# Performance work log

Hardware: AMD Instinct MI355X
Metric: run time of the kernel (lower is better)

The kernel has to match this reference:

```python
import jax, jax.numpy as jnp
import numpy as np

H = 32          # num query heads
KV = 8          # num kv heads
D = 64          # head_dim
WIN = 512       # sliding_window
BASE = 10000.0  # rope base


def setup_inputs() -> dict:
    key = jax.random.key(0)
    ks = jax.random.split(key, 5)
    B, S, DIM = 2, 2048, 2048
    x = jax.random.normal(ks[0], (B, S, DIM), dtype=jnp.float32)
    wq = jax.random.normal(ks[1], (H * D, DIM), dtype=jnp.float32) * 0.02
    wk = jax.random.normal(ks[2], (KV * D, DIM), dtype=jnp.float32) * 0.02
    wv = jax.random.normal(ks[3], (KV * D, DIM), dtype=jnp.float32) * 0.02
    wo = jax.random.normal(ks[4], (DIM, H * D), dtype=jnp.float32) * 0.02
    return {"x": x, "wq": wq, "wk": wk, "wv": wv, "wo": wo}


def _rope_tables(S):
    inv_freq = 1.0 / (BASE ** (jnp.arange(0, D, 2, dtype=jnp.float32) / D))
    t = jnp.arange(S, dtype=jnp.float32)
    freqs = t[:, None] * inv_freq[None, :]          # [S, D/2]
    emb = jnp.concatenate([freqs, freqs], axis=-1)  # [S, D]
    return jnp.cos(emb)[:, None, :], jnp.sin(emb)[:, None, :]  # [S,1,D]


def _rotate_half(u):
    return jnp.concatenate([-u[..., D // 2:], u[..., :D // 2]], axis=-1)


def reference(x, wq, wk, wv, wo):
    B, S, _ = x.shape
    q = (x @ wq.T).reshape(B, S, H, D)
    k = (x @ wk.T).reshape(B, S, KV, D)
    v = (x @ wv.T).reshape(B, S, KV, D)

    cos, sin = _rope_tables(S)  # [S,1,D] broadcasts over batch and heads
    q = q * cos + _rotate_half(q) * sin
    k = k * cos + _rotate_half(k) * sin

    q = q.transpose(0, 2, 1, 3)                        # [B,H,S,D]
    k = jnp.repeat(k.transpose(0, 2, 1, 3), H // KV, axis=1)  # [B,H,S,D]
    v = jnp.repeat(v.transpose(0, 2, 1, 3), H // KV, axis=1)

    scale = 1.0 / jnp.sqrt(jnp.float32(D))
    scores = jnp.einsum('bhqd,bhkd->bhqk', q, k) * scale  # [B,H,S,S]

    i = jnp.arange(S)[:, None]
    j = jnp.arange(S)[None, :]
    window_mask = jnp.abs(i - j) > WIN // 2   # True = masked (outside window)
    causal_mask = j > i                        # True = masked (future)
    masked = window_mask | causal_mask
    scores = jnp.where(masked[None, None], -jnp.inf, scores)

    attn = jax.nn.softmax(scores, axis=-1)
    out = jnp.einsum('bhqk,bhkd->bhqd', attn, v)  # [B,H,S,D]
    out = out.transpose(0, 2, 1, 3).reshape(B, S, H * D)
    return out @ wo.T
```

## Files before the change

### kernel.cpp

```cpp
#include <hip/hip_runtime.h>
#include <cstdint>
#include <cstddef>

#define SLEN 2048
#define NB 2
#define NH 32
#define NKV 8
#define HD 64
#define MROWS 4096
#define QDIM 2048
#define KVDIM 512
#define WINH 256

typedef float f32x4 __attribute__((ext_vector_type(4)));
typedef __bf16 bf16x8 __attribute__((ext_vector_type(8)));

__device__ __forceinline__ unsigned short f2bf(float f) {
  union { float f; unsigned u; } v; v.f = f;
  unsigned r = v.u + 0x7fffu + ((v.u >> 16) & 1u);
  return (unsigned short)(r >> 16);
}
__device__ __forceinline__ float bf2f(unsigned short h) {
  union { unsigned u; float f; } v; v.u = ((unsigned)h) << 16;
  return v.f;
}
__device__ __forceinline__ unsigned pk2(float a, float b) {
  return (unsigned)f2bf(a) | ((unsigned)f2bf(b) << 16);
}
__device__ __forceinline__ uint4 cvt16(float4 a, float4 b) {
  uint4 u;
  u.x = pk2(a.x, a.y); u.y = pk2(a.z, a.w);
  u.z = pk2(b.x, b.y); u.w = pk2(b.z, b.w);
  return u;
}
__device__ __forceinline__ void async16(const unsigned short* g, unsigned short* l) {
  __builtin_amdgcn_global_load_lds(
      (const __attribute__((address_space(1))) unsigned int*)g,
      (__attribute__((address_space(3))) unsigned int*)l, 16, 0, 0);
}

__global__ void rope_table(float2* __restrict__ tab) {
  int tid = blockIdx.x * 256 + threadIdx.x;
  int d = tid & 31;
  int s = tid >> 5;
  float inv = expf((float)d * (-2.0f / 64.0f) * 9.210340371976184f);
  float ang = (float)s * inv;
  float sn, cs;
  sincosf(ang, &sn, &cs);
  tab[tid] = make_float2(cs, sn);
}

__global__ void conv_bf16(const float* __restrict__ src, unsigned short* __restrict__ dst) {
  size_t t = (size_t)blockIdx.x * 256 + threadIdx.x;
  float4 a = *(const float4*)(src + t * 8);
  float4 b = *(const float4*)(src + t * 8 + 4);
  *(uint4*)(dst + t * 8) = cvt16(a, b);
}

__global__ void conv_wqkv(const float* __restrict__ wq, const float* __restrict__ wk,
                          const float* __restrict__ wv, unsigned short* __restrict__ dst) {
  size_t t = (size_t)blockIdx.x * 256 + threadIdx.x;
  size_t e = t * 8;
  int row = (int)(e >> 11);
  const float* src; size_t off;
  if (row < 2048)       { src = wq; off = e; }
  else if (row < 2560)  { src = wk; off = e - (size_t)2048 * 2048; }
  else                  { src = wv; off = e - (size_t)2560 * 2048; }
  float4 a = *(const float4*)(src + off);
  float4 b = *(const float4*)(src + off + 4);
  *(uint4*)(dst + e) = cvt16(a, b);
}

__global__ void rope_qk(unsigned short* __restrict__ qb,
                        unsigned short* __restrict__ kb,
                        const float* __restrict__ tabf) {
  const float2* tab = (const float2*)tabf;
  int tid = blockIdx.x * 256 + threadIdx.x;
  int oct = tid & 3;
  int head = (tid >> 2) % 40;
  int row = tid / 160;
  int s = row & (SLEN - 1);
  int d0 = oct * 8;
  unsigned short* p = (head < NH)
      ? qb + (size_t)row * QDIM + head * HD
      : kb + (size_t)row * KVDIM + (head - NH) * HD;
  uint4 u0 = *(const uint4*)(p + d0);
  uint4 u1 = *(const uint4*)(p + d0 + 32);
  const unsigned short* a16 = (const unsigned short*)&u0;
  const unsigned short* b16 = (const unsigned short*)&u1;
  unsigned short o0[8], o1[8];
#pragma unroll
  for (int j = 0; j < 8; ++j) {
    float2 cs = tab[s * 32 + d0 + j];
    float a = bf2f(a16[j]), b = bf2f(b16[j]);
    o0[j] = f2bf(a * cs.x - b * cs.y);
    o1[j] = f2bf(b * cs.x + a * cs.y);
  }
  *(uint4*)(p + d0)      = *(const uint4*)o0;
  *(uint4*)(p + d0 + 32) = *(const uint4*)o1;
}

__global__ __launch_bounds__(512, 2) void qkv_gemm(
    const unsigned short* __restrict__ Ap, const unsigned short* __restrict__ Bp,
    unsigned short* __restrict__ o_q, unsigned short* __restrict__ o_k,
    unsigned short* __restrict__ o_v)
{
  extern __shared__ unsigned short L[];
  constexpr int NT = 32;

  const int bid = blockIdx.x;
  const int swz = (bid & 7) * 32 + (bid >> 3);
  const int bm0 = (swz & 15) * 256;
  const int bn0 = (swz >> 4) * 192;

  const int tid = threadIdx.x;
  const int lane = tid & 63, wid = tid >> 6;
  const int g = lane >> 4, cl = lane & 15;
  const int wm = wid >> 2, wn = wid & 3;

  const int r0 = wid * 32 + (lane >> 2);
  const int s0 = (((lane & 3) ^ ((lane >> 3) & 3)) << 3);
  const unsigned short* gA = Ap + (size_t)(bm0 + r0) * 2048 + s0;
  const unsigned short* gB = Bp + (size_t)(bn0 + r0) * 2048 + s0;

  const int slotus = ((g ^ ((cl >> 1) & 3)) << 3);
  const int aread = (wm * 128 + cl) * 32 + slotus;
  const int bread = (wn * 48 + cl) * 32 + slotus;

#define REG_(b, op, kh) ((((b) * 2 + (op)) * 2 + (kh)) * 8192)
#define STG(op, kh, tt, db) do { \
    const unsigned short* s_ = ((op) ? gB : gA) + (tt) * 64 + (kh) * 32; \
    unsigned short* d_ = L + REG_(db, op, kh) + wid * 1024; \
    async16(s_, d_); \
    async16(s_ + 16 * 2048, d_ + 512); \
  } while (0)
#define LDA(dst, kh, mh) \
    _Pragma("unroll") for (int mf = 0; mf < 4; ++mf) \
      dst[mf] = *(const bf16x8*)&L[REG_(cb, 0, kh) + aread + (mh) * 2048 + mf * 512];
#define LDB(dst, kh) \
    _Pragma("unroll") for (int nf = 0; nf < 3; ++nf) \
      dst[nf] = *(const bf16x8*)&L[REG_(cb, 1, kh) + bread + nf * 512];
#define MM(mh, A, B) do { \
    __builtin_amdgcn_s_setprio(1); \
    _Pragma("unroll") for (int mf = 0; mf < 4; ++mf) \
      _Pragma("unroll") for (int nf = 0; nf < 3; ++nf) \
        acc[(mh) * 4 + mf][nf] = __builtin_amdgcn_mfma_f32_16x16x32_bf16( \
            A[mf], B[nf], acc[(mh) * 4 + mf][nf], 0, 0, 0); \
    __builtin_amdgcn_s_setprio(0); \
  } while (0)

  f32x4 acc[8][3] = {};

  STG(0, 0, 0, 0); STG(1, 0, 0, 0); STG(0, 1, 0, 0); STG(1, 1, 0, 0);
  STG(0, 0, 1, 1); STG(1, 0, 1, 1);
  asm volatile("s_waitcnt vmcnt(4)" ::: "memory");
  __builtin_amdgcn_s_barrier();
  __builtin_amdgcn_sched_barrier(0);

#pragma unroll 1
  for (int t = 0; t < NT; ++t) {
    const int cb = t & 1, nb = cb ^ 1;
    bf16x8 a00[4], a10[4], a01[4], a11[4], b0[3], b1[3];

    if (t + 1 < NT) STG(0, 1, t + 1, nb);
    LDA(a00, 0, 0); LDB(b0, 0);
    if (t + 1 < NT) STG(1, 1, t + 1, nb);
    LDA(a10, 0, 1);
    MM(0, a00, b0);
    LDA(a01, 1, 0); LDB(b1, 1);
    MM(1, a10, b0);
    asm volatile("s_waitcnt lgkmcnt(0)" ::: "memory");
    __builtin_amdgcn_s_barrier();
    __builtin_amdgcn_sched_barrier(0);
    if (t + 2 < NT) STG(0, 0, t + 2, cb);
    LDA(a11, 1, 1);
    MM(0, a01, b1);
    if (t + 2 < NT) STG(1, 0, t + 2, cb);
    MM(1, a11, b1);
    if (t + 2 < NT) { asm volatile("s_waitcnt vmcnt(4)" ::: "memory"); }
    else            { asm volatile("s_waitcnt vmcnt(0)" ::: "memory"); }
    asm volatile("s_waitcnt lgkmcnt(0)" ::: "memory");
    __builtin_amdgcn_s_barrier();
    __builtin_amdgcn_sched_barrier(0);
  }
#undef MM
#undef LDB
#undef LDA
#undef STG
#undef REG_

  const int rb = bm0 + wm * 128;
#pragma unroll
  for (int m = 0; m < 8; ++m)
#pragma unroll
    for (int nf = 0; nf < 3; ++nf) {
      const int col = bn0 + wn * 48 + nf * 16 + cl;
      if (col < QDIM) {
#pragma unroll
        for (int p = 0; p < 4; ++p) {
          int row = rb + m * 16 + g * 4 + p;
          o_q[(size_t)row * QDIM + col] = f2bf(acc[m][nf][p]);
        }
      } else if (col < QDIM + KVDIM) {
#pragma unroll
        for (int p = 0; p < 4; ++p) {
          int row = rb + m * 16 + g * 4 + p;
          o_k[(size_t)row * KVDIM + col - QDIM] = f2bf(acc[m][nf][p]);
        }
      } else {
        int vc = col - QDIM - KVDIM;
        int kvh = vc >> 6, d = vc & 63;
        int row0 = rb + m * 16 + g * 4;
        int bb = row0 >> 11, s = row0 & (SLEN - 1);
        unsigned short* dst = o_v + (((size_t)(bb * NKV + kvh) * HD + d) << 11) + s;
        uint2 u;
        u.x = pk2(acc[m][nf][0], acc[m][nf][1]);
        u.y = pk2(acc[m][nf][2], acc[m][nf][3]);
        *(uint2*)dst = u;
      }
    }
}

__global__ __launch_bounds__(512, 2) void out_gemm(
    const unsigned short* __restrict__ Ap, const unsigned short* __restrict__ Bp,
    float* __restrict__ o_f)
{
  extern __shared__ unsigned short L[];
  constexpr int NT = 32;

  const int bid = blockIdx.x;
  const int swz = (bid & 7) * 32 + (bid >> 3);
  const int bm0 = (swz & 31) * 128;
  const int bn0 = (swz >> 5) * 256;

  const int tid = threadIdx.x;
  const int lane = tid & 63, wid = tid >> 6;
  const int g = lane >> 4, cl = lane & 15;
  const int wm = wid >> 2, wn = wid & 3;

  const int s0 = (((lane & 3) ^ ((lane >> 3) & 3)) << 3);
  const unsigned short* gA = Ap + (size_t)(bm0 + wid * 16 + (lane >> 2)) * 2048 + s0;
  const unsigned short* gB = Bp + (size_t)(bn0 + wid * 32 + (lane >> 2)) * 2048 + s0;

  const int slotus = ((g ^ ((cl >> 1) & 3)) << 3);
  const int aread = (wm * 64 + cl) * 32 + slotus;
  const int bread = (wn * 64 + cl) * 32 + slotus;

#define REGA_(b, kh) ((b) * 24576 + (kh) * 4096)
#define REGB_(b, kh) ((b) * 24576 + 8192 + (kh) * 8192)
#define STGA(kh, tt, db) \
    async16(gA + (tt) * 64 + (kh) * 32, L + REGA_(db, kh) + wid * 512)
#define STGB(kh, tt, db) do { \
    const unsigned short* s_ = gB + (tt) * 64 + (kh) * 32; \
    unsigned short* d_ = L + REGB_(db, kh) + wid * 1024; \
    async16(s_, d_); \
    async16(s_ + 16 * 2048, d_ + 512); \
  } while (0)
#define LA(dst, kh, mp) \
    _Pragma("unroll") for (int mf = 0; mf < 2; ++mf) \
      dst[mf] = *(const bf16x8*)&L[REGA_(cb, kh) + aread + (mp) * 1024 + mf * 512];
#define LB(dst, kh) \
    _Pragma("unroll") for (int nf = 0; nf < 4; ++nf) \
      dst[nf] = *(const bf16x8*)&L[REGB_(cb, kh) + bread + nf * 512];
#define MMO(mp, A, B) do { \
    __builtin_amdgcn_s_setprio(1); \
    _Pragma("unroll") for (int mf = 0; mf < 2; ++mf) \
      _Pragma("unroll") for (int nf = 0; nf < 4; ++nf) \
        acc[(mp) * 2 + mf][nf] = __builtin_amdgcn_mfma_f32_16x16x32_bf16( \
            A[mf], B[nf], acc[(mp) * 2 + mf][nf], 0, 0, 0); \
    __builtin_amdgcn_s_setprio(0); \
  } while (0)

  f32x4 acc[4][4] = {};

  STGA(0, 0, 0); STGB(0, 0, 0); STGA(1, 0, 0); STGB(1, 0, 0);
  STGA(0, 1, 1); STGB(0, 1, 1);
  asm volatile("s_waitcnt vmcnt(3)" ::: "memory");
  __builtin_amdgcn_s_barrier();
  __builtin_amdgcn_sched_barrier(0);

#pragma unroll 1
  for (int t = 0; t < NT; ++t) {
    const int cb = t & 1, nb = cb ^ 1;
    bf16x8 p00[2], p10[2], p01[2], p11[2], b0[4], b1[4];

    if (t + 1 < NT) STGA(1, t + 1, nb);
    LA(p00, 0, 0); LB(b0, 0);
    if (t + 1 < NT) STGB(1, t + 1, nb);
    LA(p10, 0, 1);
    MMO(0, p00, b0);
    LA(p01, 1, 0); LB(b1, 1);
    MMO(1, p10, b0);
    asm volatile("s_waitcnt lgkmcnt(0)" ::: "memory");
    __builtin_amdgcn_s_barrier();
    __builtin_amdgcn_sched_barrier(0);
    if (t + 2 < NT) STGA(0, t + 2, cb);
    LA(p11, 1, 1);
    MMO(0, p01, b1);
    if (t + 2 < NT) STGB(0, t + 2, cb);
    MMO(1, p11, b1);
    if (t + 2 < NT) { asm volatile("s_waitcnt vmcnt(3)" ::: "memory"); }
    else            { asm volatile("s_waitcnt vmcnt(0)" ::: "memory"); }
    asm volatile("s_waitcnt lgkmcnt(0)" ::: "memory");
    __builtin_amdgcn_s_barrier();
    __builtin_amdgcn_sched_barrier(0);
  }
#undef MMO
#undef LB
#undef LA
#undef STGB
#undef STGA
#undef REGB_
#undef REGA_

  const int rb = bm0 + wm * 64;
  const int colb = bn0 + wn * 64;
#pragma unroll
  for (int m = 0; m < 4; ++m)
#pragma unroll
    for (int nf = 0; nf < 4; ++nf)
#pragma unroll
      for (int p = 0; p < 4; ++p) {
        int row = rb + m * 16 + g * 4 + p;
        o_f[(size_t)row * 2048 + colb + nf * 16 + cl] = acc[m][nf][p];
      }
}

__global__ __launch_bounds__(256) void attn(
    const unsigned short* __restrict__ qb, const unsigned short* __restrict__ kb,
    const unsigned short* __restrict__ vt, unsigned short* __restrict__ ao)
{
  __shared__ __align__(16) unsigned short Plds[4][16][40];
  const int lane = threadIdx.x & 63, wid = threadIdx.x >> 6;
  const int g = lane >> 4, cl = lane & 15;
  const int qt = blockIdx.x * 4 + wid;
  const int bh = qt >> 7, tl = qt & 127;
  const int i0 = tl * 16;
  const int b = bh >> 5, h = bh & 31, kvh = (bh & 31) >> 2;
  const int qi = i0 + cl;

  const unsigned short* qp = qb + ((size_t)(b * SLEN + i0 + cl) * NH + h) * HD + g * 8;
  bf16x8 qf0 = *(const bf16x8*)qp;
  bf16x8 qf1 = *(const bf16x8*)(qp + 32);

  f32x4 acc_o[4] = {};
  float m_run = -1e30f, l_run = 0.f;
  int jb = i0 - WINH; if (jb < 0) jb = 0;

  for (int j0 = jb; j0 <= i0; j0 += 32) {
    f32x4 sacc[2];
#pragma unroll
    for (int t = 0; t < 2; ++t) {
      int krow = j0 + 16 * t + cl;
      if (krow > SLEN - 1) krow = SLEN - 1;
      const unsigned short* kp = kb + ((size_t)(b * SLEN + krow) * NKV + kvh) * HD + g * 8;
      bf16x8 kf0 = *(const bf16x8*)kp;
      bf16x8 kf1 = *(const bf16x8*)(kp + 32);
      f32x4 z = {};
      z = __builtin_amdgcn_mfma_f32_16x16x32_bf16(kf0, qf0, z, 0, 0, 0);
      z = __builtin_amdgcn_mfma_f32_16x16x32_bf16(kf1, qf1, z, 0, 0, 0);
      sacc[t] = z;
    }
    float s[2][4];
    float mx = -1e30f;
#pragma unroll
    for (int t = 0; t < 2; ++t)
#pragma unroll
      for (int p = 0; p < 4; ++p) {
        int kj = j0 + 16 * t + g * 4 + p;
        bool ok = (kj <= qi) && (qi - kj <= WINH);
        float v = ok ? sacc[t][p] * 0.125f : -1e30f;
        s[t][p] = v;
        mx = fmaxf(mx, v);
      }
    mx = fmaxf(mx, __shfl_xor(mx, 16));
    mx = fmaxf(mx, __shfl_xor(mx, 32));
    float mnew = fmaxf(m_run, mx);
    float corr = __expf(m_run - mnew);
    float ps = 0.f;
    unsigned pw[2][2];
#pragma unroll
    for (int t = 0; t < 2; ++t) {
      float p0 = __expf(s[t][0] - mnew);
      float p1 = __expf(s[t][1] - mnew);
      float p2 = __expf(s[t][2] - mnew);
      float p3 = __expf(s[t][3] - mnew);
      ps += p0 + p1 + p2 + p3;
      pw[t][0] = pk2(p0, p1);
      pw[t][1] = pk2(p2, p3);
    }
    ps += __shfl_xor(ps, 16);
    ps += __shfl_xor(ps, 32);
    l_run = l_run * corr + ps;
    m_run = mnew;
#pragma unroll
    for (int vbk = 0; vbk < 4; ++vbk)
#pragma unroll
      for (int p = 0; p < 4; ++p) acc_o[vbk][p] *= corr;
#pragma unroll
    for (int t = 0; t < 2; ++t) {
      *(unsigned*)&Plds[wid][cl][16 * t + 4 * g]     = pw[t][0];
      *(unsigned*)&Plds[wid][cl][16 * t + 4 * g + 2] = pw[t][1];
    }
    bf16x8 pf = *(const bf16x8*)&Plds[wid][cl][g * 8];
    int jv = j0 + g * 8;
    if (jv > SLEN - 8) jv = SLEN - 8;
    const unsigned short* vbase = vt + ((size_t)(b * NKV + kvh) * HD) * SLEN + jv;
#pragma unroll
    for (int vbk = 0; vbk < 4; ++vbk) {
      bf16x8 vf = *(const bf16x8*)(vbase + (size_t)(vbk * 16 + cl) * SLEN);
      acc_o[vbk] = __builtin_amdgcn_mfma_f32_16x16x32_bf16(vf, pf, acc_o[vbk], 0, 0, 0);
    }
  }
  float inv = 1.0f / l_run;
  unsigned short* op = ao + ((size_t)(b * SLEN + i0 + cl) * NH + h) * HD;
#pragma unroll
  for (int vbk = 0; vbk < 4; ++vbk) {
    unsigned u0 = pk2(acc_o[vbk][0] * inv, acc_o[vbk][1] * inv);
    unsigned u1 = pk2(acc_o[vbk][2] * inv, acc_o[vbk][3] * inv);
    *(unsigned*)(op + vbk * 16 + g * 4)     = u0;
    *(unsigned*)(op + vbk * 16 + g * 4 + 2) = u1;
  }
}

extern "C" void kernel_launch(void* const* d_in, const int* in_sizes, int n_in,
                              void* d_out, int out_size, void* d_ws, size_t ws_size,
                              hipStream_t stream) {
  const float* x  = (const float*)d_in[0];
  const float* wq = (const float*)d_in[1];
  const float* wk = (const float*)d_in[2];
  const float* wv = (const float*)d_in[3];
  const float* wo = (const float*)d_in[4];
  float* out = (float*)d_out;

  char* w = (char*)d_ws;
  unsigned short* wqkvb = (unsigned short*)w; w += (size_t)3136 * 2048 * 2;
  unsigned short* xb    = (unsigned short*)w; w += (size_t)MROWS * QDIM * 2;
  unsigned short* qb    = (unsigned short*)w; w += (size_t)MROWS * QDIM * 2;
  unsigned short* kb    = (unsigned short*)w; w += (size_t)MROWS * KVDIM * 2;
  unsigned short* vt    = (unsigned short*)w; w += (size_t)MROWS * KVDIM * 2;
  float* tab            = (float*)w;          w += (size_t)SLEN * 32 * 8;
  unsigned short* wob = wqkvb;
  unsigned short* ao  = xb;

  hipFuncSetAttribute((const void*)qkv_gemm,
                      hipFuncAttributeMaxDynamicSharedMemorySize, 131072);
  hipFuncSetAttribute((const void*)out_gemm,
                      hipFuncAttributeMaxDynamicSharedMemorySize, 98304);

  rope_table<<<SLEN * 32 / 256, 256, 0, stream>>>((float2*)tab);
  conv_bf16<<<(MROWS * 2048) / (8 * 256), 256, 0, stream>>>(x, xb);
  conv_wqkv<<<(3072 * 2048) / (8 * 256), 256, 0, stream>>>(wq, wk, wv, wqkvb);
  qkv_gemm<<<256, 512, 131072, stream>>>(xb, wqkvb, qb, kb, vt);
  rope_qk<<<(MROWS * 40 * 4) / 256, 256, 0, stream>>>(qb, kb, tab);
  conv_bf16<<<(2048 * 2048) / (8 * 256), 256, 0, stream>>>(wo, wob);
  attn<<<(NB * NH * (SLEN / 16)) / 4, 256, 0, stream>>>(qb, kb, vt, ao);
  out_gemm<<<256, 512, 98304, stream>>>(ao, wob, out);
}
```

Measured before the change: 196.9 us.

## Process two query tiles per wave in attention with K prefetch double-buffering

Each attention wave now handles 32 query rows (two 16-row tiles) instead of 16, so every K and V fragment loaded from global memory feeds two sets of MFMAs. K fragments for the next 32-key block are prefetched into alternating register buffers, and bf16 packing uses the hardware v_cvt_pk_bf16_f32 instruction instead of manual rounding. Register pressure roughly doubles and the grid halves, which lowers occupancy and wave count, and each wave walks a slightly longer key range for its wider query tile.

```diff
diff --git a/kernel.cpp b/kernel.cpp
--- a/kernel.cpp
+++ b/kernel.cpp
@@ -26,6 +26,11 @@
 }
 __device__ __forceinline__ unsigned pk2(float a, float b) {
   return (unsigned)f2bf(a) | ((unsigned)f2bf(b) << 16);
+}
+__device__ __forceinline__ unsigned cvtpk(float a, float b) {
+  unsigned r;
+  asm("v_cvt_pk_bf16_f32 %0, %1, %2" : "=v"(r) : "v"(a), "v"(b));
+  return r;
 }
 __device__ __forceinline__ uint4 cvt16(float4 a, float4 b) {
   uint4 u;
@@ -330,96 +335,119 @@
     const unsigned short* __restrict__ qb, const unsigned short* __restrict__ kb,
     const unsigned short* __restrict__ vt, unsigned short* __restrict__ ao)
 {
-  __shared__ __align__(16) unsigned short Plds[4][16][40];
+  __shared__ __align__(16) unsigned short Plds[4][2][16][40];
   const int lane = threadIdx.x & 63, wid = threadIdx.x >> 6;
   const int g = lane >> 4, cl = lane & 15;
   const int qt = blockIdx.x * 4 + wid;
-  const int bh = qt >> 7, tl = qt & 127;
-  const int i0 = tl * 16;
+  const int bh = qt >> 6, tl = qt & 63;
+  const int i0 = tl * 32;
   const int b = bh >> 5, h = bh & 31, kvh = (bh & 31) >> 2;
-  const int qi = i0 + cl;
-
-  const unsigned short* qp = qb + ((size_t)(b * SLEN + i0 + cl) * NH + h) * HD + g * 8;
-  bf16x8 qf0 = *(const bf16x8*)qp;
-  bf16x8 qf1 = *(const bf16x8*)(qp + 32);
-
-  f32x4 acc_o[4] = {};
-  float m_run = -1e30f, l_run = 0.f;
-  int jb = i0 - WINH; if (jb < 0) jb = 0;
-
-  for (int j0 = jb; j0 <= i0; j0 += 32) {
-    f32x4 sacc[2];
-#pragma unroll
-    for (int t = 0; t < 2; ++t) {
-      int krow = j0 + 16 * t + cl;
-      if (krow > SLEN - 1) krow = SLEN - 1;
-      const unsigned short* kp = kb + ((size_t)(b * SLEN + krow) * NKV + kvh) * HD + g * 8;
-      bf16x8 kf0 = *(const bf16x8*)kp;
-      bf16x8 kf1 = *(const bf16x8*)(kp + 32);
-      f32x4 z = {};
-      z = __builtin_amdgcn_mfma_f32_16x16x32_bf16(kf0, qf0, z, 0, 0, 0);
-      z = __builtin_amdgcn_mfma_f32_16x16x32_bf16(kf1, qf1, z, 0, 0, 0);
-      sacc[t] = z;
-    }
-    float s[2][4];
-    float mx = -1e30f;
-#pragma unroll
-    for (int t = 0; t < 2; ++t)
-#pragma unroll
-      for (int p = 0; p < 4; ++p) {
-        int kj = j0 + 16 * t + g * 4 + p;
-        bool ok = (kj <= qi) && (qi - kj <= WINH);
-        float v = ok ? sacc[t][p] * 0.125f : -1e30f;
-        s[t][p] = v;
-        mx = fmaxf(mx, v);
-      }
-    mx = fmaxf(mx, __shfl_xor(mx, 16));
-    mx = fmaxf(mx, __shfl_xor(mx, 32));
-    float mnew = fmaxf(m_run, mx);
-    float corr = __expf(m_run - mnew);
-    float ps = 0.f;
-    unsigned pw[2][2];
-#pragma unroll
-    for (int t = 0; t < 2; ++t) {
-      float p0 = __expf(s[t][0] - mnew);
-      float p1 = __expf(s[t][1] - mnew);
-      float p2 = __expf(s[t][2] - mnew);
-      float p3 = __expf(s[t][3] - mnew);
-      ps += p0 + p1 + p2 + p3;
-      pw[t][0] = pk2(p0, p1);
-      pw[t][1] = pk2(p2, p3);
-    }
-    ps += __shfl_xor(ps, 16);
-    ps += __shfl_xor(ps, 32);
-    l_run = l_run * corr + ps;
-    m_run = mnew;
-#pragma unroll
-    for (int vbk = 0; vbk < 4; ++vbk)
-#pragma unroll
-      for (int p = 0; p < 4; ++p) acc_o[vbk][p] *= corr;
-#pragma unroll
-    for (int t = 0; t < 2; ++t) {
-      *(unsigned*)&Plds[wid][cl][16 * t + 4 * g]     = pw[t][0];
-      *(unsigned*)&Plds[wid][cl][16 * t + 4 * g + 2] = pw[t][1];
-    }
-    bf16x8 pf = *(const bf16x8*)&Plds[wid][cl][g * 8];
-    int jv = j0 + g * 8;
-    if (jv > SLEN - 8) jv = SLEN - 8;
-    const unsigned short* vbase = vt + ((size_t)(b * NKV + kvh) * HD) * SLEN + jv;
-#pragma unroll
-    for (int vbk = 0; vbk < 4; ++vbk) {
-      bf16x8 vf = *(const bf16x8*)(vbase + (size_t)(vbk * 16 + cl) * SLEN);
-      acc_o[vbk] = __builtin_amdgcn_mfma_f32_16x16x32_bf16(vf, pf, acc_o[vbk], 0, 0, 0);
-    }
+  const int qi0 = i0 + cl, qi1 = i0 + 16 + cl;
+
+  const unsigned short* qp0 = qb + ((size_t)(b * SLEN + qi0) * NH + h) * HD + g * 8;
+  const unsigned short* qp1 = qb + ((size_t)(b * SLEN + qi1) * NH + h) * HD + g * 8;
+  bf16x8 qf00 = *(const bf16x8*)qp0, qf01 = *(const bf16x8*)(qp0 + 32);
+  bf16x8 qf10 = *(const bf16x8*)qp1, qf11 = *(const bf16x8*)(qp1 + 32);
+
+  const unsigned short* kbase = kb + ((size_t)b * SLEN * NKV + kvh) * HD + g * 8;
+  const unsigned short* vbase = vt + ((size_t)(b * NKV + kvh) * HD) * SLEN;
+
+  f32x4 acc0[4] = {}, acc1[4] = {};
+  float m0 = -1e30f, l0 = 0.f, m1 = -1e30f, l1 = 0.f;
+  const int jb = (i0 > WINH) ? (i0 - WINH) : 0;
+
+#define LOADK(dst, jj) do { \
+    _Pragma("unroll") for (int t = 0; t < 2; ++t) { \
+      int krow = (jj) + 16 * t + cl; \
+      if (krow > SLEN - 1) krow = SLEN - 1; \
+      const unsigned short* kp_ = kbase + (size_t)krow * KVDIM; \
+      dst[t * 2]     = *(const bf16x8*)kp_; \
+      dst[t * 2 + 1] = *(const bf16x8*)(kp_ + 32); \
+    } \
+  } while (0)
+
+#define SOFTMAX(SAC, MR, LR, ACC, QI, QF) do { \
+    float sm[2][4]; float mx = -1e30f; \
+    _Pragma("unroll") for (int t = 0; t < 2; ++t) \
+      _Pragma("unroll") for (int p = 0; p < 4; ++p) { \
+        int kj = j0 + 16 * t + 4 * g + p; \
+        bool ok = (kj <= (QI)) && ((QI) - kj <= WINH); \
+        float v = ok ? SAC[t][p] * 0.125f : -1e30f; \
+        sm[t][p] = v; mx = fmaxf(mx, v); \
+      } \
+    mx = fmaxf(mx, __shfl_xor(mx, 16)); \
+    mx = fmaxf(mx, __shfl_xor(mx, 32)); \
+    float mnew = fmaxf(MR, mx); \
+    float corr = __expf(MR - mnew); \
+    float ps = 0.f; unsigned pw00, pw01, pw10, pw11; \
+    { \
+      float p0 = __expf(sm[0][0] - mnew), p1 = __expf(sm[0][1] - mnew); \
+      float p2 = __expf(sm[0][2] - mnew), p3 = __expf(sm[0][3] - mnew); \
+      ps += p0 + p1 + p2 + p3; pw00 = cvtpk(p0, p1); pw01 = cvtpk(p2, p3); \
+      float p4 = __expf(sm[1][0] - mnew), p5 = __expf(sm[1][1] - mnew); \
+      float p6 = __expf(sm[1][2] - mnew), p7 = __expf(sm[1][3] - mnew); \
+      ps += p4 + p5 + p6 + p7; pw10 = cvtpk(p4, p5); pw11 = cvtpk(p6, p7); \
+    } \
+    ps += __shfl_xor(ps, 16); ps += __shfl_xor(ps, 32); \
+    LR = LR * corr + ps; MR = mnew; \
+    _Pragma("unroll") for (int vb2 = 0; vb2 < 4; ++vb2) \
+      _Pragma("unroll") for (int p = 0; p < 4; ++p) ACC[vb2][p] *= corr; \
+    *(unsigned*)&Plds[wid][QF][cl][4 * g]          = pw00; \
+    *(unsigned*)&Plds[wid][QF][cl][4 * g + 2]      = pw01; \
+    *(unsigned*)&Plds[wid][QF][cl][16 + 4 * g]     = pw10; \
+    *(unsigned*)&Plds[wid][QF][cl][16 + 4 * g + 2] = pw11; \
+  } while (0)
+
+#define BODY(CUR, NXT) do { \
+    LOADK(NXT, j0 + 32);                          \
+    bf16x8 vf[4]; \
+    { \
+      int jv = j0 + g * 8; \
+      if (jv > SLEN - 8) jv = SLEN - 8; \
+      _Pragma("unroll") for (int vb2 = 0; vb2 < 4; ++vb2) \
+        vf[vb2] = *(const bf16x8*)(vbase + (size_t)(vb2 * 16 + cl) * SLEN + jv); \
+    } \
+    f32x4 s0[2], s1[2]; \
+    _Pragma("unroll") for (int t = 0; t < 2; ++t) { \
+      f32x4 z = {}; \
+      z = __builtin_amdgcn_mfma_f32_16x16x32_bf16(CUR[t * 2], qf00, z, 0, 0, 0); \
+      z = __builtin_amdgcn_mfma_f32_16x16x32_bf16(CUR[t * 2 + 1], qf01, z, 0, 0, 0); \
+      s0[t] = z; \
+      f32x4 z2 = {}; \
+      z2 = __builtin_amdgcn_mfma_f32_16x16x32_bf16(CUR[t * 2], qf10, z2, 0, 0, 0); \
+      z2 = __builtin_amdgcn_mfma_f32_16x16x32_bf16(CUR[t * 2 + 1], qf11, z2, 0, 0, 0); \
+      s1[t] = z2; \
+    } \
+    SOFTMAX(s0, m0, l0, acc0, qi0, 0); \
+    SOFTMAX(s1, m1, l1, acc1, qi1, 1); \
+    bf16x8 pf0 = *(const bf16x8*)&Plds[wid][0][cl][g * 8]; \
+    bf16x8 pf1 = *(const bf16x8*)&Plds[wid][1][cl][g * 8]; \
+    _Pragma("unroll") for (int vb2 = 0; vb2 < 4; ++vb2) \
+      acc0[vb2] = __builtin_amdgcn_mfma_f32_16x16x32_bf16(vf[vb2], pf0, acc0[vb2], 0, 0, 0); \
+    _Pragma("unroll") for (int vb2 = 0; vb2 < 4; ++vb2) \
+      acc1[vb2] = __builtin_amdgcn_mfma_f32_16x16x32_bf16(vf[vb2], pf1, acc1[vb2], 0, 0, 0); \
+  } while (0)
+
+  bf16x8 kA[4], kB[4];
+  LOADK(kA, jb);
+  int j0 = jb;
+  for (;;) {
+    BODY(kA, kB); j0 += 32; if (j0 > i0) break;
+    BODY(kB, kA); j0 += 32; if (j0 > i0) break;
   }
-  float inv = 1.0f / l_run;
-  unsigned short* op = ao + ((size_t)(b * SLEN + i0 + cl) * NH + h) * HD;
+#undef BODY
+#undef SOFTMAX
+#undef LOADK
+
+  float inv0 = 1.0f / l0, inv1 = 1.0f / l1;
+  unsigned short* op0 = ao + ((size_t)(b * SLEN + qi0) * NH + h) * HD;
+  unsigned short* op1 = ao + ((size_t)(b * SLEN + qi1) * NH + h) * HD;
 #pragma unroll
   for (int vbk = 0; vbk < 4; ++vbk) {
-    unsigned u0 = pk2(acc_o[vbk][0] * inv, acc_o[vbk][1] * inv);
-    unsigned u1 = pk2(acc_o[vbk][2] * inv, acc_o[vbk][3] * inv);
-    *(unsigned*)(op + vbk * 16 + g * 4)     = u0;
-    *(unsigned*)(op + vbk * 16 + g * 4 + 2) = u1;
+    *(unsigned*)(op0 + vbk * 16 + g * 4)     = cvtpk(acc0[vbk][0] * inv0, acc0[vbk][1] * inv0);
+    *(unsigned*)(op0 + vbk * 16 + g * 4 + 2) = cvtpk(acc0[vbk][2] * inv0, acc0[vbk][3] * inv0);
+    *(unsigned*)(op1 + vbk * 16 + g * 4)     = cvtpk(acc1[vbk][0] * inv1, acc1[vbk][1] * inv1);
+    *(unsigned*)(op1 + vbk * 16 + g * 4 + 2) = cvtpk(acc1[vbk][2] * inv1, acc1[vbk][3] * inv1);
   }
 }
 
@@ -454,6 +482,6 @@
   qkv_gemm<<<256, 512, 131072, stream>>>(xb, wqkvb, qb, kb, vt);
   rope_qk<<<(MROWS * 40 * 4) / 256, 256, 0, stream>>>(qb, kb, tab);
   conv_bf16<<<(2048 * 2048) / (8 * 256), 256, 0, stream>>>(wo, wob);
-  attn<<<(NB * NH * (SLEN / 16)) / 4, 256, 0, stream>>>(qb, kb, vt, ao);
+  attn<<<(NB * NH * (SLEN / 32)) / 4, 256, 0, stream>>>(qb, kb, vt, ao);
   out_gemm<<<256, 512, 98304, stream>>>(ao, wob, out);
 }
```

Result: faster. 168.8 us (-14.3%).
